# Performance work log

Hardware: AMD Instinct MI355X
Metric: run time of the kernel (lower is better)

The kernel has to match this reference:

```python
import jax, jax.numpy as jnp
import numpy as np

H = 128; L = 4; N_TOTAL = 2500; M = 4; K = 12
S = N_TOTAL * M          # 10000 subgraphs
F = S * K                # 120000 flat nodes
E_INTRA = 2 * F          # 240000 intra-subgraph edges
E_INTER = 16 * N_TOTAL   # 40000 canonical edges
B = 50; VOCAB = 119; MAX_DIST = 32; BN_EPS = 1e-5


def _bn(x, g, b):
    # training-mode BatchNorm1d over rows (biased var, eps=1e-5)
    mu = x.mean(0)
    var = x.var(0)
    return (x - mu) * jax.lax.rsqrt(var + BN_EPS) * g + b


def _gine(x, ei, ea, W1, b1, W2, b2):
    # PyG GINEConv, eps=0: MLP(x + sum_{src->dst} relu(x[src] + e))
    msg = jax.nn.relu(x[ei[0]] + ea)                              # [E,H]
    agg = jax.ops.segment_sum(msg, ei[1], num_segments=x.shape[0])
    h = x + agg
    return jax.nn.relu(h @ W1 + b1) @ W2 + b2


def setup_inputs():
    key = jax.random.key(0)
    ks = list(jax.random.split(key, 32)); it = iter(ks)
    nk = lambda: next(it)
    rn = lambda shape, s=0.05: jax.random.normal(nk(), shape, dtype=jnp.float32) * s
    x_tok = jax.random.randint(nk(), (F,), 0, VOCAB)
    dist = jax.random.randint(nk(), (F,), 0, MAX_DIST + 1)
    node_ids = jax.random.randint(nk(), (F,), 0, N_TOTAL)
    node_ids = jnp.where(jax.random.uniform(nk(), (F,)) < 0.1, -1, node_ids)
    root_flat_idx = jnp.arange(S) * K
    node_ids = node_ids.at[root_flat_idx].set(jnp.arange(S) // M)  # root = canonical node
    valid = node_ids >= 0
    sub_batch = jnp.repeat(jnp.arange(S), K)
    src = jax.random.randint(nk(), (E_INTRA,), 0, F)
    dst = (src // K) * K + jax.random.randint(nk(), (E_INTRA,), 0, K)  # stay inside subgraph
    intra_ei = jnp.stack([src, dst])
    edge_index = jax.random.randint(nk(), (2, E_INTER), 0, N_TOTAL)
    batch_ids = jnp.arange(N_TOTAL) // (N_TOTAL // B)
    lp = -jax.random.uniform(nk(), (S,)) * 3.0                    # log-probs <= 0
    z = lambda *shape: jnp.zeros(shape, jnp.float32)
    o = lambda *shape: jnp.ones(shape, jnp.float32)
    return dict(
        x_tok=x_tok, dist=dist, node_ids=node_ids, valid=valid,
        sub_batch=sub_batch, root_flat_idx=root_flat_idx,
        intra_ei=intra_ei, edge_index=edge_index, batch_ids=batch_ids,
        lp=lp, ea_flat=rn((E_INTRA, H)), edge_attr=rn((E_INTER, H)),
        atom_emb=rn((VOCAB, H)), dist_emb=rn((MAX_DIST + 1, H)),
        logp_w=rn((1, H)), logp_b=z(H),
        intra_W1=rn((L, H, H)), intra_b1=z(L, H),
        intra_W2=rn((L, H, H)), intra_b2=z(L, H),
        intra_bn_g=o(L, H), intra_bn_b=z(L, H),
        self_W=rn((L, H, H)), self_b=z(L, H),
        root_W=rn((L, H, H)), root_b=z(L, H),
        inter_W1=rn((L, H, H)), inter_b1=z(L, H),
        inter_W2=rn((L, H, H)), inter_b2=z(L, H),
        inter_bn_g=o(L, H), inter_bn_b=z(L, H),
        readout_bn_g=o(H), readout_bn_b=z(H),
        alpha_pool=o(1), alpha_inter=o(1),
    )


def reference(x_tok, dist, node_ids, valid, sub_batch, root_flat_idx, intra_ei,
              edge_index, batch_ids, lp, ea_flat, edge_attr, atom_emb, dist_emb,
              logp_w, logp_b, intra_W1, intra_b1, intra_W2, intra_b2,
              intra_bn_g, intra_bn_b, self_W, self_b, root_W, root_b,
              inter_W1, inter_b1, inter_W2, inter_b2, inter_bn_g, inter_bn_b,
              readout_bn_g, readout_bn_b, alpha_pool, alpha_inter):
    valid_f = valid.astype(jnp.float32)[:, None]                  # [F,1]
    is_root_f = jnp.zeros((F, 1), jnp.float32).at[root_flat_idx].set(1.0)
    clamped_ids = jnp.maximum(node_ids, 0)
    # input encoding: atom embedding + BFS-distance PE + log-prob PE
    logp_pe = jax.nn.relu(lp[sub_batch][:, None] * logp_w[0] + logp_b)
    h = (atom_emb[x_tok] + dist_emb[dist] + logp_pe) * valid_f
    # HT inter-root weights, normalized per canonical root id
    root_ids = node_ids[root_flat_idx]                            # [S]
    rv = root_ids >= 0
    rid = jnp.maximum(root_ids, 0)
    w_un = jnp.where(rv, jnp.exp(-alpha_inter[0] * lp), 0.0)
    w_sum = jax.ops.segment_sum(w_un, rid, num_segments=N_TOTAL)
    ht_w = jnp.where(rv, w_un / (w_sum[rid] + 1e-16), 0.0)        # [S]
    for l in range(L):
        h1 = _gine(h, intra_ei, ea_flat, intra_W1[l], intra_b1[l], intra_W2[l], intra_b2[l])
        h1 = _bn(h1, intra_bn_g[l], intra_bn_b[l]) * valid_f
        h_root_bcast = h[sub_batch * K]
        h_non_root = (h @ self_W[l] + self_b[l]) + (h_root_bcast @ root_W[l] + root_b[l])
        # HT-weighted scatter of root reps to canonical nodes
        h_roots = h[root_flat_idx]                                # [S,H]
        h_root_canon = jax.ops.segment_sum(h_roots * ht_w[:, None], rid, num_segments=N_TOTAL)
        h_inter = _gine(h_root_canon, edge_index, edge_attr, inter_W1[l], inter_b1[l], inter_W2[l], inter_b2[l])
        h_inter = _bn(h_inter, inter_bn_g[l], inter_bn_b[l])
        h_inter_bcast = h_inter[clamped_ids] * valid_f
        out = is_root_f * (h1 + h_inter_bcast) + (1.0 - is_root_f) * (h1 + h_non_root)
        h = jax.nn.relu(out) * valid_f                            # dropout p=0
    # HT softmax readout over the m subgraphs of each canonical node
    h_sub = jax.ops.segment_sum(h * valid_f, sub_batch, num_segments=S)
    h_sub_2d = h_sub.reshape(N_TOTAL, M, H)
    w = jax.nn.softmax(-alpha_pool[0] * lp.reshape(N_TOTAL, M), axis=1)
    node_emb = jnp.einsum('nm,nmh->nh', w, h_sub_2d)
    node_emb = _bn(node_emb, readout_bn_g, readout_bn_b)
    return jax.ops.segment_sum(node_emb, batch_ids, num_segments=B)  # [B,H]
```

## Files before the change

kernel.cpp:

```cpp
#include <hip/hip_runtime.h>
#include <math.h>

#define H 128
#define H4 (H/4)
#define KK 12
#define MSUB 4
#define FF 120000
#define SS 10000
#define NN 2500
#define NBATCH 50
#define NLAYER 4
#define EINTRA 240000
#define EINTER 40000
#define HH (H*H)
#define BN_EPS 1e-5f
#define CAP_I 32
#define CAP_E 96
#define WLO_SHORTS 16384

typedef short short8 __attribute__((ext_vector_type(8)));
typedef float floatx4 __attribute__((ext_vector_type(4)));

__device__ __forceinline__ unsigned short f2bf_rne(float x){
  unsigned u = __float_as_uint(x);
  unsigned r = u + 0x7FFFu + ((u >> 16) & 1u);
  return (unsigned short)(r >> 16);
}


__global__ void k_zeroi(int* __restrict__ p, int n){
  int i = blockIdx.x*256 + threadIdx.x;
  if (i < n) p[i] = 0;
}


__global__ void k_bucket(const int* __restrict__ dst, int E, int* __restrict__ cnt,
                         int* __restrict__ beid, int cap){
  int e = blockIdx.x*256 + threadIdx.x;
  if (e >= E) return;
  int d = dst[e];
  int p = atomicAdd(&cnt[d], 1);
  if (p < cap) beid[(size_t)d*cap + p] = e;
}

__global__ void k_scan(const int* __restrict__ cnt, int rows, int cap,
                       int* __restrict__ rowptr, int* __restrict__ gcount){
  __shared__ int sdata[256];
  __shared__ int sbase;
  int tid = threadIdx.x;
  int r = blockIdx.x*256 + tid;
  int v = 0;
  if (r < rows){ v = cnt[r]; if (v > cap) v = cap; }
  sdata[tid] = v;
  __syncthreads();
  for (int ofs = 1; ofs < 256; ofs <<= 1){
    int t = (tid >= ofs) ? sdata[tid-ofs] : 0;
    __syncthreads();
    sdata[tid] += t;
    __syncthreads();
  }
  if (tid == 255) sbase = atomicAdd(gcount, sdata[255]);
  __syncthreads();
  if (r < rows) rowptr[r] = sbase + sdata[tid] - v;
}

__global__ void k_csr_fill(const int* __restrict__ cnt, const int* __restrict__ rowptr,
                           const int* __restrict__ beid, const int* __restrict__ src,
                           int rows, int cap, int2* __restrict__ es){
  int f = blockIdx.x*256 + threadIdx.x;
  if (f >= rows) return;
  int n = cnt[f]; if (n > cap) n = cap;
  int base = rowptr[f];
  const int* bl = beid + (size_t)f*cap;
  for (int i = 0; i < n; ++i){
    int e = bl[i];
    es[base + i] = make_int2(e, src[e]);
  }
}


__global__ void k_wprep(const float* __restrict__ iW1, const float* __restrict__ iW2,
                        const float* __restrict__ sW,  const float* __restrict__ rW,
                        const float* __restrict__ nW1, const float* __restrict__ nW2,
                        short* __restrict__ wlo){
  int mat = blockIdx.x >> 3;
  int t = (blockIdx.x & 7)*256 + threadIdx.x;
  int l = t & 63, nt = (t >> 6) & 7, ks = t >> 9;
  int layer = mat / 6, which = mat % 6;
  const float* W;
  switch (which){
    case 0: W = iW1; break; case 1: W = iW2; break; case 2: W = sW; break;
    case 3: W = rW;  break; case 4: W = nW1; break; default: W = nW2; break;
  }
  W += (size_t)layer*HH;
  short* o = wlo + (size_t)mat*WLO_SHORTS;
  int quad = l >> 4, n15 = l & 15;
  #pragma unroll
  for (int j = 0; j < 8; ++j){
    int k = ks*32 + quad*8 + j;
    int n = nt*16 + n15;
    float v = W[(size_t)k*H + n];
    unsigned short hb = f2bf_rne(v);
    float hf = __uint_as_float((unsigned)hb << 16);
    o[(ks*8 + nt)*512 + l*8 + j] = (short)f2bf_rne(v - hf);
  }
}


__global__ void k_encode(float* __restrict__ h, const int* __restrict__ xtok,
                         const int* __restrict__ dist, const int* __restrict__ nids,
                         const int* __restrict__ subb, const float* __restrict__ lp,
                         const float* __restrict__ aemb, const float* __restrict__ demb,
                         const float* __restrict__ lw, const float* __restrict__ lb){
  int idx = blockIdx.x*256 + threadIdx.x;
  if (idx >= FF*H4) return;
  int f = idx >> 5; int c = (idx & 31) << 2;
  float vf = (nids[f] >= 0) ? 1.f : 0.f;
  float l = lp[subb[f]];
  float4 a = *(const float4*)(aemb + (size_t)xtok[f]*H + c);
  float4 d = *(const float4*)(demb + (size_t)dist[f]*H + c);
  float4 w = *(const float4*)(lw + c);
  float4 b = *(const float4*)(lb + c);
  float4 o;
  o.x = (a.x + d.x + fmaxf(fmaf(l, w.x, b.x), 0.f)) * vf;
  o.y = (a.y + d.y + fmaxf(fmaf(l, w.y, b.y), 0.f)) * vf;
  o.z = (a.z + d.z + fmaxf(fmaf(l, w.z, b.z), 0.f)) * vf;
  o.w = (a.w + d.w + fmaxf(fmaf(l, w.w, b.w), 0.f)) * vf;
  *(float4*)(h + (size_t)f*H + c) = o;
}


__global__ void k_htw(const int* __restrict__ nids, const int* __restrict__ rfi,
                      const float* __restrict__ lp, const float* __restrict__ alpha,
                      float* __restrict__ htw){
  int n = blockIdx.x*256 + threadIdx.x;
  if (n >= NN) return;
  float a = alpha[0];
  float w[MSUB]; float sum = 0.f;
  #pragma unroll
  for (int m = 0; m < MSUB; ++m){
    int s = n*MSUB + m;
    int rid = nids[rfi[s]];
    float wm = (rid >= 0) ? expf(-a*lp[s]) : 0.f;
    w[m] = wm; sum += wm;
  }
  float inv = 1.f / (sum + 1e-16f);
  #pragma unroll
  for (int m = 0; m < MSUB; ++m) htw[n*MSUB + m] = w[m]*inv;
}


__global__ void k_gine_gather2(float* __restrict__ outa, const float* __restrict__ x,
                               const float* __restrict__ ea, const int* __restrict__ cnt,
                               const int* __restrict__ rowptr, const int2* __restrict__ es,
                               int rows, int cap){
  int idx = blockIdx.x*256 + threadIdx.x;
  if (idx >= rows*H4) return;
  int f = idx >> 5; int c = (idx & 31) << 2;
  float4 acc = *(const float4*)(x + (size_t)f*H + c);
  int n = cnt[f]; if (n > cap) n = cap;
  const int2* p = es + rowptr[f];
  int i = 0;
  for (; i + 2 <= n; i += 2){
    int2 e0 = p[i];
    int2 e1 = p[i+1];
    float4 x0 = *(const float4*)(x + (size_t)e0.y*H + c);
    float4 a0 = *(const float4*)(ea + (size_t)e0.x*H + c);
    float4 x1 = *(const float4*)(x + (size_t)e1.y*H + c);
    float4 a1 = *(const float4*)(ea + (size_t)e1.x*H + c);
    acc.x += fmaxf(x0.x + a0.x, 0.f) + fmaxf(x1.x + a1.x, 0.f);
    acc.y += fmaxf(x0.y + a0.y, 0.f) + fmaxf(x1.y + a1.y, 0.f);
    acc.z += fmaxf(x0.z + a0.z, 0.f) + fmaxf(x1.z + a1.z, 0.f);
    acc.w += fmaxf(x0.w + a0.w, 0.f) + fmaxf(x1.w + a1.w, 0.f);
  }
  if (i < n){
    int2 e0 = p[i];
    float4 x0 = *(const float4*)(x + (size_t)e0.y*H + c);
    float4 a0 = *(const float4*)(ea + (size_t)e0.x*H + c);
    acc.x += fmaxf(x0.x + a0.x, 0.f);
    acc.y += fmaxf(x0.y + a0.y, 0.f);
    acc.z += fmaxf(x0.z + a0.z, 0.f);
    acc.w += fmaxf(x0.w + a0.w, 0.f);
  }
  *(float4*)(outa + (size_t)f*H + c) = acc;
}


__global__ void k_canon(float* __restrict__ canon, const float* __restrict__ h,
                        const float* __restrict__ htw, const int* __restrict__ rfi){
  int idx = blockIdx.x*256 + threadIdx.x;
  if (idx >= NN*H4) return;
  int n = idx >> 5; int c = (idx & 31) << 2;
  float4 acc = make_float4(0.f,0.f,0.f,0.f);
  #pragma unroll
  for (int m = 0; m < MSUB; ++m){
    int s = n*MSUB + m;
    float w = htw[s];
    const float* p = h + (size_t)rfi[s]*H + c;
    acc.x += w*p[0]; acc.y += w*p[1]; acc.z += w*p[2]; acc.w += w*p[3];
  }
  *(float4*)(canon + (size_t)n*H + c) = acc;
}


__global__ __launch_bounds__(256, 2) void k_mm_mfma(
    const float* __restrict__ in, float* __restrict__ out, int rows,
    const float* __restrict__ W, const short* __restrict__ wlo,
    const float* __restrict__ bias, int do_relu, const int* __restrict__ gather)
{
  __shared__ __align__(16) short whi[4][8][64][8];
  int tid = threadIdx.x;
  int w = tid >> 6, l = tid & 63;
  int quad = l >> 4, n15 = l & 15;

  #pragma unroll
  for (int i = 0; i < 8; ++i){
    int c = w + (i << 2);
    int ks = c >> 3, nt = c & 7;
    #pragma unroll
    for (int j = 0; j < 8; ++j){
      int k = ks*32 + quad*8 + j;
      int n = nt*16 + n15;
      whi[ks][nt][l][j] = (short)f2bf_rne(W[(size_t)k*H + n]);
    }
  }
  __syncthreads();

  const short* wlol = wlo + l*8;

  int ngroups = (rows + 63) >> 6;
  for (int g = blockIdx.x; g < ngroups; g += gridDim.x){
    int rload = g*64 + w*16 + n15;
    bool okload = rload < rows;
    int ir = okload ? (gather ? gather[rload] : rload) : 0;
    const float* ap = in + (size_t)ir*H + quad*8;

    short8 ah[4], al[4];
    #pragma unroll
    for (int ks = 0; ks < 4; ++ks){
      float4 a0 = okload ? *(const float4*)(ap + ks*32 + 0) : make_float4(0.f,0.f,0.f,0.f);
      float4 a1 = okload ? *(const float4*)(ap + ks*32 + 4) : make_float4(0.f,0.f,0.f,0.f);
      float av[8] = {a0.x,a0.y,a0.z,a0.w,a1.x,a1.y,a1.z,a1.w};
      #pragma unroll
      for (int j = 0; j < 8; ++j){
        unsigned short hb = f2bf_rne(av[j]);
        float hf = __uint_as_float((unsigned)hb << 16);
        ah[ks][j] = (short)hb;
        al[ks][j] = (short)f2bf_rne(av[j] - hf);
      }
    }

    floatx4 acc[8] = {};
    #pragma unroll
    for (int ks = 0; ks < 4; ++ks){
      #pragma unroll
      for (int nt = 0; nt < 8; ++nt){
        short8 bh = *(const short8*)&whi[ks][nt][l][0];
        short8 bl = *(const short8*)(wlol + (ks*8 + nt)*512);
        acc[nt] = __builtin_amdgcn_mfma_f32_16x16x32_bf16(ah[ks], bh, acc[nt], 0, 0, 0);
        acc[nt] = __builtin_amdgcn_mfma_f32_16x16x32_bf16(al[ks], bh, acc[nt], 0, 0, 0);
        acc[nt] = __builtin_amdgcn_mfma_f32_16x16x32_bf16(ah[ks], bl, acc[nt], 0, 0, 0);
      }
    }

    int rbase = g*64 + w*16 + quad*4;
    #pragma unroll
    for (int nt = 0; nt < 8; ++nt){
      int col = nt*16 + n15;
      float bv = bias[col];
      #pragma unroll
      for (int reg = 0; reg < 4; ++reg){
        int r = rbase + reg;
        if (r < rows){
          float v = acc[nt][reg] + bv;
          if (do_relu) v = fmaxf(v, 0.f);
          out[(size_t)r*H + col] = v;
        }
      }
    }
  }
}


__global__ __launch_bounds__(256, 2) void k_mm_mfma_stats(
    const float* __restrict__ in, float* __restrict__ out, int rows,
    const float* __restrict__ W, const short* __restrict__ wlo,
    const float* __restrict__ bias, double* __restrict__ part)
{
  __shared__ __align__(16) short whi[4][8][64][8];
  int tid = threadIdx.x;
  int w = tid >> 6, l = tid & 63;
  int quad = l >> 4, n15 = l & 15;

  #pragma unroll
  for (int i = 0; i < 8; ++i){
    int c = w + (i << 2);
    int ks = c >> 3, nt = c & 7;
    #pragma unroll
    for (int j = 0; j < 8; ++j){
      int k = ks*32 + quad*8 + j;
      int n = nt*16 + n15;
      whi[ks][nt][l][j] = (short)f2bf_rne(W[(size_t)k*H + n]);
    }
  }
  __syncthreads();

  const short* wlol = wlo + l*8;

  float s0[8] = {0,0,0,0,0,0,0,0};
  float s1[8] = {0,0,0,0,0,0,0,0};

  int ngroups = (rows + 63) >> 6;
  for (int g = blockIdx.x; g < ngroups; g += gridDim.x){
    int rload = g*64 + w*16 + n15;
    bool okload = rload < rows;
    const float* ap = in + (size_t)(okload ? rload : 0)*H + quad*8;

    short8 ah[4], al[4];
    #pragma unroll
    for (int ks = 0; ks < 4; ++ks){
      float4 a0 = okload ? *(const float4*)(ap + ks*32 + 0) : make_float4(0.f,0.f,0.f,0.f);
      float4 a1 = okload ? *(const float4*)(ap + ks*32 + 4) : make_float4(0.f,0.f,0.f,0.f);
      float av[8] = {a0.x,a0.y,a0.z,a0.w,a1.x,a1.y,a1.z,a1.w};
      #pragma unroll
      for (int j = 0; j < 8; ++j){
        unsigned short hb = f2bf_rne(av[j]);
        float hf = __uint_as_float((unsigned)hb << 16);
        ah[ks][j] = (short)hb;
        al[ks][j] = (short)f2bf_rne(av[j] - hf);
      }
    }

    floatx4 acc[8] = {};
    #pragma unroll
    for (int ks = 0; ks < 4; ++ks){
      #pragma unroll
      for (int nt = 0; nt < 8; ++nt){
        short8 bh = *(const short8*)&whi[ks][nt][l][0];
        short8 bl = *(const short8*)(wlol + (ks*8 + nt)*512);
        acc[nt] = __builtin_amdgcn_mfma_f32_16x16x32_bf16(ah[ks], bh, acc[nt], 0, 0, 0);
        acc[nt] = __builtin_amdgcn_mfma_f32_16x16x32_bf16(al[ks], bh, acc[nt], 0, 0, 0);
        acc[nt] = __builtin_amdgcn_mfma_f32_16x16x32_bf16(ah[ks], bl, acc[nt], 0, 0, 0);
      }
    }

    int rbase = g*64 + w*16 + quad*4;
    #pragma unroll
    for (int nt = 0; nt < 8; ++nt){
      int col = nt*16 + n15;
      float bv = bias[col];
      #pragma unroll
      for (int reg = 0; reg < 4; ++reg){
        int r = rbase + reg;
        if (r < rows){
          float v = acc[nt][reg] + bv;
          out[(size_t)r*H + col] = v;
          s0[nt] += v;
          s1[nt] += v*v;
        }
      }
    }
  }

  __syncthreads();
  double* red = (double*)&whi[0][0][0][0];
  #pragma unroll
  for (int nt = 0; nt < 8; ++nt){
    float a = s0[nt], b = s1[nt];
    a += __shfl_xor(a, 16, 64); b += __shfl_xor(b, 16, 64);
    a += __shfl_xor(a, 32, 64); b += __shfl_xor(b, 32, 64);
    if (quad == 0){
      int col = nt*16 + n15;
      red[(size_t)(w*2+0)*H + col] = (double)a;
      red[(size_t)(w*2+1)*H + col] = (double)b;
    }
  }
  __syncthreads();
  if (tid < H){
    int col = tid;
    double a = red[0*H+col] + red[2*H+col] + red[4*H+col] + red[6*H+col];
    double b = red[1*H+col] + red[3*H+col] + red[5*H+col] + red[7*H+col];
    part[(size_t)(blockIdx.x*2+0)*H + col] = a;
    part[(size_t)(blockIdx.x*2+1)*H + col] = b;
  }
}


__global__ void k_bnstats_p(const float* __restrict__ x, int rows, double* __restrict__ part){
  int g = blockIdx.x*256 + threadIdx.x;
  int c = g & (H-1);
  int s = g >> 7;
  int stride = (gridDim.x*256) >> 7;
  double a = 0.0, b = 0.0;
  for (int r = s; r < rows; r += stride){
    float v = x[(size_t)r*H + c];
    a += v; b += (double)v*(double)v;
  }
  part[(size_t)(s*2+0)*H + c] = a;
  part[(size_t)(s*2+1)*H + c] = b;
}

__global__ void k_bnfin_par(const double* __restrict__ part, int nstreams, int rows,
                            float* __restrict__ muinv){
  __shared__ double sh0[256], sh1[256];
  int c = blockIdx.x;
  int tid = threadIdx.x;
  double a = 0.0, b = 0.0;
  for (int s = tid; s < nstreams; s += 256){
    a += part[(size_t)(s*2+0)*H + c];
    b += part[(size_t)(s*2+1)*H + c];
  }
  sh0[tid] = a; sh1[tid] = b;
  __syncthreads();
  for (int ofs = 128; ofs > 0; ofs >>= 1){
    if (tid < ofs){ sh0[tid] += sh0[tid+ofs]; sh1[tid] += sh1[tid+ofs]; }
    __syncthreads();
  }
  if (tid == 0){
    double mu = sh0[0] / (double)rows;
    double var = sh1[0] / (double)rows - mu*mu;
    muinv[c]   = (float)mu;
    muinv[H+c] = (float)(1.0 / sqrt(var + (double)BN_EPS));
  }
}

__global__ void k_bnapply(float* __restrict__ x, const float* __restrict__ muinv,
                          const float* __restrict__ g, const float* __restrict__ b, int rows){
  int idx = blockIdx.x*256 + threadIdx.x;
  if (idx >= rows*H4) return;
  int r = idx >> 5; int c = (idx & 31) << 2;
  float4 v  = *(const float4*)(x + (size_t)r*H + c);
  float4 mu = *(const float4*)(muinv + c);
  float4 iv = *(const float4*)(muinv + H + c);
  float4 gg = *(const float4*)(g + c);
  float4 bb = *(const float4*)(b + c);
  v.x = (v.x-mu.x)*iv.x*gg.x + bb.x;
  v.y = (v.y-mu.y)*iv.y*gg.y + bb.y;
  v.z = (v.z-mu.z)*iv.z*gg.z + bb.z;
  v.w = (v.w-mu.w)*iv.w*gg.w + bb.w;
  *(float4*)(x + (size_t)r*H + c) = v;
}


__global__ void k_combine(float* __restrict__ h, const float* __restrict__ h1raw,
                          const float* __restrict__ r1, const float* __restrict__ r2,
                          const float* __restrict__ hinter, const float* __restrict__ muinv,
                          const float* __restrict__ bg, const float* __restrict__ bb,
                          const int* __restrict__ nids){
  int idx = blockIdx.x*256 + threadIdx.x;
  if (idx >= FF*H4) return;
  int f = idx >> 5; int c = (idx & 31) << 2;
  int nid = nids[f];
  float vf = (nid >= 0) ? 1.f : 0.f;
  int cid = (nid < 0) ? 0 : nid;
  float4 x  = *(const float4*)(h1raw + (size_t)f*H + c);
  float4 mu = *(const float4*)(muinv + c);
  float4 iv = *(const float4*)(muinv + H + c);
  float4 g4 = *(const float4*)(bg + c);
  float4 b4 = *(const float4*)(bb + c);
  float4 h1;
  h1.x = ((x.x-mu.x)*iv.x*g4.x + b4.x) * vf;
  h1.y = ((x.y-mu.y)*iv.y*g4.y + b4.y) * vf;
  h1.z = ((x.z-mu.z)*iv.z*g4.z + b4.z) * vf;
  h1.w = ((x.w-mu.w)*iv.w*g4.w + b4.w) * vf;
  float4 o;
  if (f % KK == 0){
    float4 hi = *(const float4*)(hinter + (size_t)cid*H + c);
    o.x = h1.x + hi.x*vf; o.y = h1.y + hi.y*vf; o.z = h1.z + hi.z*vf; o.w = h1.w + hi.w*vf;
  } else {
    float4 a  = *(const float4*)(r1 + (size_t)f*H + c);
    float4 rr = *(const float4*)(r2 + (size_t)(f/KK)*H + c);
    o.x = h1.x + a.x + rr.x; o.y = h1.y + a.y + rr.y; o.z = h1.z + a.z + rr.z; o.w = h1.w + a.w + rr.w;
  }
  o.x = fmaxf(o.x,0.f)*vf; o.y = fmaxf(o.y,0.f)*vf; o.z = fmaxf(o.z,0.f)*vf; o.w = fmaxf(o.w,0.f)*vf;
  *(float4*)(h + (size_t)f*H + c) = o;
}


__global__ void k_hsub(float* __restrict__ hsub, const float* __restrict__ h){
  int idx = blockIdx.x*256 + threadIdx.x;
  if (idx >= SS*H4) return;
  int s = idx >> 5; int c = (idx & 31) << 2;
  float4 acc = make_float4(0.f,0.f,0.f,0.f);
  const float* base = h + (size_t)s*KK*H + c;
  #pragma unroll
  for (int k = 0; k < KK; ++k){
    float4 v = *(const float4*)(base + (size_t)k*H);
    acc.x += v.x; acc.y += v.y; acc.z += v.z; acc.w += v.w;
  }
  *(float4*)(hsub + (size_t)s*H + c) = acc;
}

__global__ void k_poolw(float* __restrict__ poolw, const float* __restrict__ lp,
                        const float* __restrict__ alpha){
  int n = blockIdx.x*256 + threadIdx.x;
  if (n >= NN) return;
  float a = alpha[0];
  float s0 = -a*lp[n*MSUB+0], s1 = -a*lp[n*MSUB+1], s2 = -a*lp[n*MSUB+2], s3 = -a*lp[n*MSUB+3];
  float m = fmaxf(fmaxf(s0,s1), fmaxf(s2,s3));
  float e0 = expf(s0-m), e1 = expf(s1-m), e2 = expf(s2-m), e3 = expf(s3-m);
  float sum = e0+e1+e2+e3;
  poolw[n*MSUB+0] = e0/sum; poolw[n*MSUB+1] = e1/sum;
  poolw[n*MSUB+2] = e2/sum; poolw[n*MSUB+3] = e3/sum;
}

__global__ void k_nodeemb(float* __restrict__ nemb, const float* __restrict__ hsub,
                          const float* __restrict__ poolw){
  int idx = blockIdx.x*256 + threadIdx.x;
  if (idx >= NN*H4) return;
  int n = idx >> 5; int c = (idx & 31) << 2;
  float w0 = poolw[n*MSUB+0], w1 = poolw[n*MSUB+1], w2 = poolw[n*MSUB+2], w3 = poolw[n*MSUB+3];
  const float* base = hsub + (size_t)n*MSUB*H + c;
  float4 v0 = *(const float4*)(base + 0*H);
  float4 v1 = *(const float4*)(base + 1*H);
  float4 v2 = *(const float4*)(base + 2*H);
  float4 v3 = *(const float4*)(base + 3*H);
  float4 o;
  o.x = w0*v0.x + w1*v1.x + w2*v2.x + w3*v3.x;
  o.y = w0*v0.y + w1*v1.y + w2*v2.y + w3*v3.y;
  o.z = w0*v0.z + w1*v1.z + w2*v2.z + w3*v3.z;
  o.w = w0*v0.w + w1*v1.w + w2*v2.w + w3*v3.w;
  *(float4*)(nemb + (size_t)n*H + c) = o;
}

__global__ void k_out(float* __restrict__ out, const float* __restrict__ nemb,
                      const float* __restrict__ muinv, const float* __restrict__ g,
                      const float* __restrict__ b){
  int idx = blockIdx.x*256 + threadIdx.x;
  if (idx >= NBATCH*H) return;
  int bi = idx >> 7; int c = idx & (H-1);
  float mu = muinv[c], iv = muinv[H+c], gg = g[c], bb = b[c];
  float acc = 0.f;
  const float* base = nemb + (size_t)bi*(NN/NBATCH)*H + c;
  for (int i = 0; i < NN/NBATCH; ++i)
    acc += (base[(size_t)i*H] - mu)*iv*gg + bb;
  out[idx] = acc;
}


extern "C" void kernel_launch(void* const* d_in, const int* in_sizes, int n_in,
                              void* d_out, int out_size, void* d_ws, size_t ws_size,
                              hipStream_t stream) {
  const int*   x_tok      = (const int*)  d_in[0];
  const int*   dist       = (const int*)  d_in[1];
  const int*   node_ids   = (const int*)  d_in[2];
  const int*   sub_batch  = (const int*)  d_in[4];
  const int*   rfi        = (const int*)  d_in[5];
  const int*   intra_ei   = (const int*)  d_in[6];
  const int*   edge_index = (const int*)  d_in[7];
  const float* lp         = (const float*)d_in[9];
  const float* ea_flat    = (const float*)d_in[10];
  const float* edge_attr  = (const float*)d_in[11];
  const float* atom_emb   = (const float*)d_in[12];
  const float* dist_emb   = (const float*)d_in[13];
  const float* logp_w     = (const float*)d_in[14];
  const float* logp_b     = (const float*)d_in[15];
  const float* intra_W1   = (const float*)d_in[16];
  const float* intra_b1   = (const float*)d_in[17];
  const float* intra_W2   = (const float*)d_in[18];
  const float* intra_b2   = (const float*)d_in[19];
  const float* intra_bn_g = (const float*)d_in[20];
  const float* intra_bn_b = (const float*)d_in[21];
  const float* self_W     = (const float*)d_in[22];
  const float* self_b     = (const float*)d_in[23];
  const float* root_W     = (const float*)d_in[24];
  const float* root_b     = (const float*)d_in[25];
  const float* inter_W1   = (const float*)d_in[26];
  const float* inter_b1   = (const float*)d_in[27];
  const float* inter_W2   = (const float*)d_in[28];
  const float* inter_b2   = (const float*)d_in[29];
  const float* inter_bn_g = (const float*)d_in[30];
  const float* inter_bn_b = (const float*)d_in[31];
  const float* ro_bn_g    = (const float*)d_in[32];
  const float* ro_bn_b    = (const float*)d_in[33];
  const float* alpha_pool = (const float*)d_in[34];
  const float* alpha_inter= (const float*)d_in[35];

  const int* isrc = intra_ei;
  const int* idst = intra_ei + EINTRA;
  const int* esrc = edge_index;
  const int* edst = edge_index + EINTER;

  float* out = (float*)d_out;

  char* ws = (char*)d_ws;
  size_t off = 0;
  auto nxt = [&](size_t bytes) -> void* {
    void* p = ws + off;
    off += (bytes + 255) & ~(size_t)255;
    return p;
  };
  const int G_MM_F = 1024;
  const int G_MM_S = (SS + 63)/64;
  const int G_MM_N = (NN + 63)/64;
  const int G_BN_S = 32;

  float*  h      = (float*) nxt((size_t)FF*H*4);
  float*  hmid   = (float*) nxt((size_t)FF*H*4);
  float*  tbuf   = (float*) nxt((size_t)FF*H*4);
  float*  r2     = (float*) nxt((size_t)SS*H*4);
  float*  canon  = (float*) nxt((size_t)NN*H*4);
  float*  agg2   = (float*) nxt((size_t)NN*H*4);
  float*  hsub   = (float*) nxt((size_t)SS*H*4);
  float*  nemb   = (float*) nxt((size_t)NN*H*4);
  float*  htw    = (float*) nxt((size_t)SS*4);
  float*  poolw  = (float*) nxt((size_t)NN*MSUB*4);
  double* statsA = (double*)nxt((size_t)G_MM_F*2*H*8);
  double* statsB = (double*)nxt((size_t)(G_BN_S*2)*2*H*8);
  float*  muinvA = (float*) nxt((size_t)2*H*4);
  float*  muinvB = (float*) nxt((size_t)2*H*4);
  short*  wloG   = (short*) nxt((size_t)24*WLO_SHORTS*2);
  int*    icnt   = (int*)   nxt((size_t)FF*4);
  int*    ibeid  = (int*)   nxt((size_t)FF*CAP_I*4);
  int*    ecnt   = (int*)   nxt((size_t)NN*4);
  int*    ebeid  = (int*)   nxt((size_t)NN*CAP_E*4);
  int*    irow   = (int*)   nxt((size_t)FF*4);
  int*    erow   = (int*)   nxt((size_t)NN*4);
  int2*   ies    = (int2*)  nxt((size_t)EINTRA*8);
  int2*   ees    = (int2*)  nxt((size_t)EINTER*8);
  int*    gcnt   = (int*)   nxt((size_t)2*4);
  (void)ws_size; (void)n_in; (void)in_sizes; (void)out_size; (void)sub_batch;

  const int G_FH4 = FF*H4/256;
  const int G_SH4 = SS*H4/256;
  const int G_NH4 = (NN*H4 + 255)/256;
  const int G_N   = (NN + 255)/256;
  const int G_F   = (FF + 255)/256;

  k_zeroi<<<G_F, 256, 0, stream>>>(icnt, FF);
  k_zeroi<<<G_N, 256, 0, stream>>>(ecnt, NN);
  k_zeroi<<<1, 256, 0, stream>>>(gcnt, 2);

  k_wprep<<<24*8, 256, 0, stream>>>(intra_W1, intra_W2, self_W, root_W,
                                    inter_W1, inter_W2, wloG);

  k_bucket<<<(EINTRA+255)/256, 256, 0, stream>>>(idst, EINTRA, icnt, ibeid, CAP_I);
  k_bucket<<<(EINTER+255)/256, 256, 0, stream>>>(edst, EINTER, ecnt, ebeid, CAP_E);
  k_scan<<<G_F, 256, 0, stream>>>(icnt, FF, CAP_I, irow, gcnt);
  k_scan<<<G_N, 256, 0, stream>>>(ecnt, NN, CAP_E, erow, gcnt+1);
  k_csr_fill<<<G_F, 256, 0, stream>>>(icnt, irow, ibeid, isrc, FF, CAP_I, ies);
  k_csr_fill<<<G_N, 256, 0, stream>>>(ecnt, erow, ebeid, esrc, NN, CAP_E, ees);

  k_encode<<<G_FH4, 256, 0, stream>>>(h, x_tok, dist, node_ids, sub_batch, lp,
                                      atom_emb, dist_emb, logp_w, logp_b);
  k_htw<<<G_N, 256, 0, stream>>>(node_ids, rfi, lp, alpha_inter, htw);

  for (int l = 0; l < NLAYER; ++l){
    const float* W1 = intra_W1 + (size_t)l*HH;
    const float* W2 = intra_W2 + (size_t)l*HH;
    const short* lo_iW1 = wloG + (size_t)(l*6+0)*WLO_SHORTS;
    const short* lo_iW2 = wloG + (size_t)(l*6+1)*WLO_SHORTS;
    const short* lo_sW  = wloG + (size_t)(l*6+2)*WLO_SHORTS;
    const short* lo_rW  = wloG + (size_t)(l*6+3)*WLO_SHORTS;
    const short* lo_nW1 = wloG + (size_t)(l*6+4)*WLO_SHORTS;
    const short* lo_nW2 = wloG + (size_t)(l*6+5)*WLO_SHORTS;

    k_gine_gather2<<<G_FH4, 256, 0, stream>>>(hmid, h, ea_flat, icnt, irow, ies, FF, CAP_I);
    k_mm_mfma<<<G_MM_F, 256, 0, stream>>>(hmid, tbuf, FF, W1, lo_iW1,
                                          intra_b1 + (size_t)l*H, 1, nullptr);
    k_mm_mfma_stats<<<G_MM_F, 256, 0, stream>>>(tbuf, hmid, FF, W2, lo_iW2,
                                                intra_b2 + (size_t)l*H, statsA);
    k_bnfin_par<<<H, 256, 0, stream>>>(statsA, G_MM_F, FF, muinvA);

    k_canon<<<G_NH4, 256, 0, stream>>>(canon, h, htw, rfi);
    k_mm_mfma<<<G_MM_S, 256, 0, stream>>>(h, r2, SS, root_W + (size_t)l*HH, lo_rW,
                                          root_b + (size_t)l*H, 0, rfi);

    k_gine_gather2<<<G_NH4, 256, 0, stream>>>(agg2, canon, edge_attr, ecnt, erow, ees, NN, CAP_E);
    k_mm_mfma<<<G_MM_N, 256, 0, stream>>>(agg2, tbuf, NN, inter_W1 + (size_t)l*HH, lo_nW1,
                                          inter_b1 + (size_t)l*H, 1, nullptr);
    k_mm_mfma<<<G_MM_N, 256, 0, stream>>>(tbuf, agg2, NN, inter_W2 + (size_t)l*HH, lo_nW2,
                                          inter_b2 + (size_t)l*H, 0, nullptr);
    k_bnstats_p<<<G_BN_S, 256, 0, stream>>>(agg2, NN, statsB);
    k_bnfin_par<<<H, 256, 0, stream>>>(statsB, G_BN_S*2, NN, muinvB);
    k_bnapply<<<G_NH4, 256, 0, stream>>>(agg2, muinvB, inter_bn_g + (size_t)l*H,
                                         inter_bn_b + (size_t)l*H, NN);

    k_mm_mfma<<<G_MM_F, 256, 0, stream>>>(h, tbuf, FF, self_W + (size_t)l*HH, lo_sW,
                                          self_b + (size_t)l*H, 0, nullptr);
    k_combine<<<G_FH4, 256, 0, stream>>>(h, hmid, tbuf, r2, agg2, muinvA,
                                         intra_bn_g + (size_t)l*H,
                                         intra_bn_b + (size_t)l*H, node_ids);
  }

  k_hsub<<<G_SH4, 256, 0, stream>>>(hsub, h);
  k_poolw<<<G_N, 256, 0, stream>>>(poolw, lp, alpha_pool);
  k_nodeemb<<<G_NH4, 256, 0, stream>>>(nemb, hsub, poolw);
  k_bnstats_p<<<G_BN_S, 256, 0, stream>>>(nemb, NN, statsB);
  k_bnfin_par<<<H, 256, 0, stream>>>(statsB, G_BN_S*2, NN, muinvB);
  k_out<<<(NBATCH*H+255)/256, 256, 0, stream>>>(out, nemb, muinvB, ro_bn_g, ro_bn_b);
}
```

Measured before the change: 2.060 ms.

## Precompute bf16 hi weight fragments and stage GEMM output through LDS for coalesced stores

The weight-prep kernel now writes both the bf16 high and low fragments in MFMA layout. Each GEMM block then fills its LDS with a straight vectorized copy instead of a strided fp32 read followed by conversion. GEMM outputs are staged per wave in a padded LDS tile and written as coalesced float4 row segments, replacing the earlier scattered scalar stores. The large-GEMM grid shrinks from 1024 to 768 blocks. The cost is extra LDS per block, which may hurt occupancy, and a second weight-fragment buffer.

Result: no change. 2.066 ms (+0.3%).

```diff
diff --git a/kernel.cpp b/kernel.cpp
--- a/kernel.cpp
+++ b/kernel.cpp
@@ -16,7 +16,8 @@
 #define BN_EPS 1e-5f
 #define CAP_I 32
 #define CAP_E 96
-#define WLO_SHORTS 16384
+#define WF_SHORTS 16384
+#define ZP 68
 
 typedef short short8 __attribute__((ext_vector_type(8)));
 typedef float floatx4 __attribute__((ext_vector_type(4)));
@@ -82,7 +83,7 @@
 __global__ void k_wprep(const float* __restrict__ iW1, const float* __restrict__ iW2,
                         const float* __restrict__ sW,  const float* __restrict__ rW,
                         const float* __restrict__ nW1, const float* __restrict__ nW2,
-                        short* __restrict__ wlo){
+                        short* __restrict__ whiG, short* __restrict__ wloG){
   int mat = blockIdx.x >> 3;
   int t = (blockIdx.x & 7)*256 + threadIdx.x;
   int l = t & 63, nt = (t >> 6) & 7, ks = t >> 9;
@@ -93,7 +94,8 @@
     case 3: W = rW;  break; case 4: W = nW1; break; default: W = nW2; break;
   }
   W += (size_t)layer*HH;
-  short* o = wlo + (size_t)mat*WLO_SHORTS;
+  short* oh = whiG + (size_t)mat*WF_SHORTS;
+  short* ol = wloG + (size_t)mat*WF_SHORTS;
   int quad = l >> 4, n15 = l & 15;
   #pragma unroll
   for (int j = 0; j < 8; ++j){
@@ -102,7 +104,9 @@
     float v = W[(size_t)k*H + n];
     unsigned short hb = f2bf_rne(v);
     float hf = __uint_as_float((unsigned)hb << 16);
-    o[(ks*8 + nt)*512 + l*8 + j] = (short)f2bf_rne(v - hf);
+    int idx = (ks*8 + nt)*512 + l*8 + j;
+    oh[idx] = (short)hb;
+    ol[idx] = (short)f2bf_rne(v - hf);
   }
 }
 
@@ -203,30 +207,36 @@
 }
 
 
+__device__ __forceinline__ void conv8(const float* av, short8& ah, short8& al){
+  #pragma unroll
+  for (int j = 0; j < 8; ++j){
+    unsigned short hb = f2bf_rne(av[j]);
+    float hf = __uint_as_float((unsigned)hb << 16);
+    ah[j] = (short)hb;
+    al[j] = (short)f2bf_rne(av[j] - hf);
+  }
+}
+
+
 __global__ __launch_bounds__(256, 2) void k_mm_mfma(
     const float* __restrict__ in, float* __restrict__ out, int rows,
-    const float* __restrict__ W, const short* __restrict__ wlo,
+    const short* __restrict__ whiG, const short* __restrict__ wlo,
     const float* __restrict__ bias, int do_relu, const int* __restrict__ gather)
 {
-  __shared__ __align__(16) short whi[4][8][64][8];
+  __shared__ __align__(16) short whi[WF_SHORTS];
+  __shared__ __align__(16) float zb[4][16][ZP];
   int tid = threadIdx.x;
   int w = tid >> 6, l = tid & 63;
   int quad = l >> 4, n15 = l & 15;
 
   #pragma unroll
-  for (int i = 0; i < 8; ++i){
-    int c = w + (i << 2);
-    int ks = c >> 3, nt = c & 7;
-    #pragma unroll
-    for (int j = 0; j < 8; ++j){
-      int k = ks*32 + quad*8 + j;
-      int n = nt*16 + n15;
-      whi[ks][nt][l][j] = (short)f2bf_rne(W[(size_t)k*H + n]);
-    }
-  }
+  for (int i = 0; i < 8; ++i)
+    *(short8*)&whi[(tid*8 + i*2048)*1] = *(const short8*)&whiG[(tid + i*256)*8];
   __syncthreads();
 
-  const short* wlol = wlo + l*8;
+  const short* hp = whi + l*8;
+  const short* lp = wlo + l*8;
+  float (*Z)[ZP] = zb[w];
 
   int ngroups = (rows + 63) >> 6;
   for (int g = blockIdx.x; g < ngroups; g += gridDim.x){
@@ -241,13 +251,7 @@
       float4 a0 = okload ? *(const float4*)(ap + ks*32 + 0) : make_float4(0.f,0.f,0.f,0.f);
       float4 a1 = okload ? *(const float4*)(ap + ks*32 + 4) : make_float4(0.f,0.f,0.f,0.f);
       float av[8] = {a0.x,a0.y,a0.z,a0.w,a1.x,a1.y,a1.z,a1.w};
-      #pragma unroll
-      for (int j = 0; j < 8; ++j){
-        unsigned short hb = f2bf_rne(av[j]);
-        float hf = __uint_as_float((unsigned)hb << 16);
-        ah[ks][j] = (short)hb;
-        al[ks][j] = (short)f2bf_rne(av[j] - hf);
-      }
+      conv8(av, ah[ks], al[ks]);
     }
 
     floatx4 acc[8] = {};
@@ -255,26 +259,39 @@
     for (int ks = 0; ks < 4; ++ks){
       #pragma unroll
       for (int nt = 0; nt < 8; ++nt){
-        short8 bh = *(const short8*)&whi[ks][nt][l][0];
-        short8 bl = *(const short8*)(wlol + (ks*8 + nt)*512);
+        short8 bh = *(const short8*)(hp + (ks*8 + nt)*512);
+        short8 bl = *(const short8*)(lp + (ks*8 + nt)*512);
         acc[nt] = __builtin_amdgcn_mfma_f32_16x16x32_bf16(ah[ks], bh, acc[nt], 0, 0, 0);
         acc[nt] = __builtin_amdgcn_mfma_f32_16x16x32_bf16(al[ks], bh, acc[nt], 0, 0, 0);
         acc[nt] = __builtin_amdgcn_mfma_f32_16x16x32_bf16(ah[ks], bl, acc[nt], 0, 0, 0);
       }
     }
 
-    int rbase = g*64 + w*16 + quad*4;
+    int rbase = g*64 + w*16;
     #pragma unroll
-    for (int nt = 0; nt < 8; ++nt){
-      int col = nt*16 + n15;
-      float bv = bias[col];
+    for (int half = 0; half < 2; ++half){
       #pragma unroll
-      for (int reg = 0; reg < 4; ++reg){
-        int r = rbase + reg;
-        if (r < rows){
+      for (int ntl = 0; ntl < 4; ++ntl){
+        int nt = half*4 + ntl;
+        float bv = bias[nt*16 + n15];
+        #pragma unroll
+        for (int reg = 0; reg < 4; ++reg){
           float v = acc[nt][reg] + bv;
           if (do_relu) v = fmaxf(v, 0.f);
-          out[(size_t)r*H + col] = v;
+          Z[quad*4 + reg][ntl*16 + n15] = v;
+        }
+      }
+      #pragma unroll
+      for (int ii = 0; ii < 2; ++ii){
+        int row = (l >> 3) + 8*ii;
+        int r = rbase + row;
+        if (r < rows){
+          float* orow = out + (size_t)r*H + half*64;
+          #pragma unroll
+          for (int jj = 0; jj < 2; ++jj){
+            int c4 = ((l & 7) + 8*jj)*4;
+            *(float4*)(orow + c4) = *(const float4*)&Z[row][c4];
+          }
         }
       }
     }
@@ -284,28 +301,23 @@
 
 __global__ __launch_bounds__(256, 2) void k_mm_mfma_stats(
     const float* __restrict__ in, float* __restrict__ out, int rows,
-    const float* __restrict__ W, const short* __restrict__ wlo,
+    const short* __restrict__ whiG, const short* __restrict__ wlo,
     const float* __restrict__ bias, double* __restrict__ part)
 {
-  __shared__ __align__(16) short whi[4][8][64][8];
+  __shared__ __align__(16) short whi[WF_SHORTS];
+  __shared__ __align__(16) float zb[4][16][ZP];
   int tid = threadIdx.x;
   int w = tid >> 6, l = tid & 63;
   int quad = l >> 4, n15 = l & 15;
 
   #pragma unroll
-  for (int i = 0; i < 8; ++i){
-    int c = w + (i << 2);
-    int ks = c >> 3, nt = c & 7;
-    #pragma unroll
-    for (int j = 0; j < 8; ++j){
-      int k = ks*32 + quad*8 + j;
-      int n = nt*16 + n15;
-      whi[ks][nt][l][j] = (short)f2bf_rne(W[(size_t)k*H + n]);
-    }
-  }
+  for (int i = 0; i < 8; ++i)
+    *(short8*)&whi[(tid*8 + i*2048)*1] = *(const short8*)&whiG[(tid + i*256)*8];
   __syncthreads();
 
-  const short* wlol = wlo + l*8;
+  const short* hp = whi + l*8;
+  const short* lp = wlo + l*8;
+  float (*Z)[ZP] = zb[w];
 
   float s0[8] = {0,0,0,0,0,0,0,0};
   float s1[8] = {0,0,0,0,0,0,0,0};
@@ -322,13 +334,7 @@
       float4 a0 = okload ? *(const float4*)(ap + ks*32 + 0) : make_float4(0.f,0.f,0.f,0.f);
       float4 a1 = okload ? *(const float4*)(ap + ks*32 + 4) : make_float4(0.f,0.f,0.f,0.f);
       float av[8] = {a0.x,a0.y,a0.z,a0.w,a1.x,a1.y,a1.z,a1.w};
-      #pragma unroll
-      for (int j = 0; j < 8; ++j){
-        unsigned short hb = f2bf_rne(av[j]);
-        float hf = __uint_as_float((unsigned)hb << 16);
-        ah[ks][j] = (short)hb;
-        al[ks][j] = (short)f2bf_rne(av[j] - hf);
-      }
+      conv8(av, ah[ks], al[ks]);
     }
 
     floatx4 acc[8] = {};
@@ -336,34 +342,46 @@
     for (int ks = 0; ks < 4; ++ks){
       #pragma unroll
       for (int nt = 0; nt < 8; ++nt){
-        short8 bh = *(const short8*)&whi[ks][nt][l][0];
-        short8 bl = *(const short8*)(wlol + (ks*8 + nt)*512);
+        short8 bh = *(const short8*)(hp + (ks*8 + nt)*512);
+        short8 bl = *(const short8*)(lp + (ks*8 + nt)*512);
         acc[nt] = __builtin_amdgcn_mfma_f32_16x16x32_bf16(ah[ks], bh, acc[nt], 0, 0, 0);
         acc[nt] = __builtin_amdgcn_mfma_f32_16x16x32_bf16(al[ks], bh, acc[nt], 0, 0, 0);
         acc[nt] = __builtin_amdgcn_mfma_f32_16x16x32_bf16(ah[ks], bl, acc[nt], 0, 0, 0);
       }
     }
 
-    int rbase = g*64 + w*16 + quad*4;
+    int rbase = g*64 + w*16;
     #pragma unroll
-    for (int nt = 0; nt < 8; ++nt){
-      int col = nt*16 + n15;
-      float bv = bias[col];
+    for (int half = 0; half < 2; ++half){
       #pragma unroll
-      for (int reg = 0; reg < 4; ++reg){
-        int r = rbase + reg;
+      for (int ntl = 0; ntl < 4; ++ntl){
+        int nt = half*4 + ntl;
+        float bv = bias[nt*16 + n15];
+        #pragma unroll
+        for (int reg = 0; reg < 4; ++reg){
+          float v = acc[nt][reg] + bv;
+          if (rbase + quad*4 + reg < rows){ s0[nt] += v; s1[nt] += v*v; }
+          Z[quad*4 + reg][ntl*16 + n15] = v;
+        }
+      }
+      #pragma unroll
+      for (int ii = 0; ii < 2; ++ii){
+        int row = (l >> 3) + 8*ii;
+        int r = rbase + row;
         if (r < rows){
-          float v = acc[nt][reg] + bv;
-          out[(size_t)r*H + col] = v;
-          s0[nt] += v;
-          s1[nt] += v*v;
+          float* orow = out + (size_t)r*H + half*64;
+          #pragma unroll
+          for (int jj = 0; jj < 2; ++jj){
+            int c4 = ((l & 7) + 8*jj)*4;
+            *(float4*)(orow + c4) = *(const float4*)&Z[row][c4];
+          }
         }
       }
     }
   }
 
   __syncthreads();
-  double* red = (double*)&whi[0][0][0][0];
+  double* red = (double*)&zb[0][0][0];
   #pragma unroll
   for (int nt = 0; nt < 8; ++nt){
     float a = s0[nt], b = s1[nt];
@@ -590,7 +608,7 @@
     off += (bytes + 255) & ~(size_t)255;
     return p;
   };
-  const int G_MM_F = 1024;
+  const int G_MM_F = 768;
   const int G_MM_S = (SS + 63)/64;
   const int G_MM_N = (NN + 63)/64;
   const int G_BN_S = 32;
@@ -609,7 +627,8 @@
   double* statsB = (double*)nxt((size_t)(G_BN_S*2)*2*H*8);
   float*  muinvA = (float*) nxt((size_t)2*H*4);
   float*  muinvB = (float*) nxt((size_t)2*H*4);
-  short*  wloG   = (short*) nxt((size_t)24*WLO_SHORTS*2);
+  short*  whiG   = (short*) nxt((size_t)24*WF_SHORTS*2);
+  short*  wloG   = (short*) nxt((size_t)24*WF_SHORTS*2);
   int*    icnt   = (int*)   nxt((size_t)FF*4);
   int*    ibeid  = (int*)   nxt((size_t)FF*CAP_I*4);
   int*    ecnt   = (int*)   nxt((size_t)NN*4);
@@ -632,7 +651,7 @@
   k_zeroi<<<1, 256, 0, stream>>>(gcnt, 2);
 
   k_wprep<<<24*8, 256, 0, stream>>>(intra_W1, intra_W2, self_W, root_W,
-                                    inter_W1, inter_W2, wloG);
+                                    inter_W1, inter_W2, whiG, wloG);
 
   k_bucket<<<(EINTRA+255)/256, 256, 0, stream>>>(idst, EINTRA, icnt, ibeid, CAP_I);
   k_bucket<<<(EINTER+255)/256, 256, 0, stream>>>(edst, EINTER, ecnt, ebeid, CAP_E);
@@ -646,37 +665,41 @@
   k_htw<<<G_N, 256, 0, stream>>>(node_ids, rfi, lp, alpha_inter, htw);
 
   for (int l = 0; l < NLAYER; ++l){
-    const float* W1 = intra_W1 + (size_t)l*HH;
-    const float* W2 = intra_W2 + (size_t)l*HH;
-    const short* lo_iW1 = wloG + (size_t)(l*6+0)*WLO_SHORTS;
-    const short* lo_iW2 = wloG + (size_t)(l*6+1)*WLO_SHORTS;
-    const short* lo_sW  = wloG + (size_t)(l*6+2)*WLO_SHORTS;
-    const short* lo_rW  = wloG + (size_t)(l*6+3)*WLO_SHORTS;
-    const short* lo_nW1 = wloG + (size_t)(l*6+4)*WLO_SHORTS;
-    const short* lo_nW2 = wloG + (size_t)(l*6+5)*WLO_SHORTS;
+    const short* hi_iW1 = whiG + (size_t)(l*6+0)*WF_SHORTS;
+    const short* hi_iW2 = whiG + (size_t)(l*6+1)*WF_SHORTS;
+    const short* hi_sW  = whiG + (size_t)(l*6+2)*WF_SHORTS;
+    const short* hi_rW  = whiG + (size_t)(l*6+3)*WF_SHORTS;
+    const short* hi_nW1 = whiG + (size_t)(l*6+4)*WF_SHORTS;
+    const short* hi_nW2 = whiG + (size_t)(l*6+5)*WF_SHORTS;
+    const short* lo_iW1 = wloG + (size_t)(l*6+0)*WF_SHORTS;
+    const short* lo_iW2 = wloG + (size_t)(l*6+1)*WF_SHORTS;
+    const short* lo_sW  = wloG + (size_t)(l*6+2)*WF_SHORTS;
+    const short* lo_rW  = wloG + (size_t)(l*6+3)*WF_SHORTS;
+    const short* lo_nW1 = wloG + (size_t)(l*6+4)*WF_SHORTS;
+    const short* lo_nW2 = wloG + (size_t)(l*6+5)*WF_SHORTS;
 
     k_gine_gather2<<<G_FH4, 256, 0, stream>>>(hmid, h, ea_flat, icnt, irow, ies, FF, CAP_I);
-    k_mm_mfma<<<G_MM_F, 256, 0, stream>>>(hmid, tbuf, FF, W1, lo_iW1,
+    k_mm_mfma<<<G_MM_F, 256, 0, stream>>>(hmid, tbuf, FF, hi_iW1, lo_iW1,
                                           intra_b1 + (size_t)l*H, 1, nullptr);
-    k_mm_mfma_stats<<<G_MM_F, 256, 0, stream>>>(tbuf, hmid, FF, W2, lo_iW2,
+    k_mm_mfma_stats<<<G_MM_F, 256, 0, stream>>>(tbuf, hmid, FF, hi_iW2, lo_iW2,
                                                 intra_b2 + (size_t)l*H, statsA);
     k_bnfin_par<<<H, 256, 0, stream>>>(statsA, G_MM_F, FF, muinvA);
 
     k_canon<<<G_NH4, 256, 0, stream>>>(canon, h, htw, rfi);
-    k_mm_mfma<<<G_MM_S, 256, 0, stream>>>(h, r2, SS, root_W + (size_t)l*HH, lo_rW,
+    k_mm_mfma<<<G_MM_S, 256, 0, stream>>>(h, r2, SS, hi_rW, lo_rW,
                                           root_b + (size_t)l*H, 0, rfi);
 
     k_gine_gather2<<<G_NH4, 256, 0, stream>>>(agg2, canon, edge_attr, ecnt, erow, ees, NN, CAP_E);
-    k_mm_mfma<<<G_MM_N, 256, 0, stream>>>(agg2, tbuf, NN, inter_W1 + (size_t)l*HH, lo_nW1,
+    k_mm_mfma<<<G_MM_N, 256, 0, stream>>>(agg2, tbuf, NN, hi_nW1, lo_nW1,
                                           inter_b1 + (size_t)l*H, 1, nullptr);
-    k_mm_mfma<<<G_MM_N, 256, 0, stream>>>(tbuf, agg2, NN, inter_W2 + (size_t)l*HH, lo_nW2,
+    k_mm_mfma<<<G_MM_N, 256, 0, stream>>>(tbuf, agg2, NN, hi_nW2, lo_nW2,
                                           inter_b2 + (size_t)l*H, 0, nullptr);
     k_bnstats_p<<<G_BN_S, 256, 0, stream>>>(agg2, NN, statsB);
     k_bnfin_par<<<H, 256, 0, stream>>>(statsB, G_BN_S*2, NN, muinvB);
     k_bnapply<<<G_NH4, 256, 0, stream>>>(agg2, muinvB, inter_bn_g + (size_t)l*H,
                                          inter_bn_b + (size_t)l*H, NN);
 
-    k_mm_mfma<<<G_MM_F, 256, 0, stream>>>(h, tbuf, FF, self_W + (size_t)l*HH, lo_sW,
+    k_mm_mfma<<<G_MM_F, 256, 0, stream>>>(h, tbuf, FF, hi_sW, lo_sW,
                                           self_b + (size_t)l*H, 0, nullptr);
     k_combine<<<G_FH4, 256, 0, stream>>>(h, hmid, tbuf, r2, agg2, muinvA,
                                          intra_bn_g + (size_t)l*H,
```
